# Kernel optimization log

Measured on AMD Instinct MI355X. Metric: run time of the kernel, lower is better.

Reference implementation:

```python
import jax, jax.numpy as jnp
import numpy as np

N_NODES = 100000
N_EDGES = 800000
IN_DIM, HID_DIM, OUT_DIM = 128, 64, 7


def setup_inputs() -> dict:
    key = jax.random.key(0)
    ks = jax.random.split(key, 8)
    x = jax.random.normal(ks[0], (N_NODES, IN_DIM), dtype=jnp.float32)
    edge_index = jax.random.randint(ks[1], (2, N_EDGES), 0, N_NODES, dtype=jnp.int64)
    # Glorot-ish init for weights, zeros for bias (PyG GCNConv default)
    def glorot(k, shape):
        lim = float(np.sqrt(6.0 / (shape[0] + shape[1])))
        return jax.random.uniform(k, shape, dtype=jnp.float32, minval=-lim, maxval=lim)
    return {
        "x": x,
        "edge_index": edge_index,
        "W1": glorot(ks[2], (IN_DIM, HID_DIM)),
        "b1": jnp.zeros((HID_DIM,), jnp.float32),
        "W2": glorot(ks[3], (HID_DIM, HID_DIM)),
        "b2": jnp.zeros((HID_DIM,), jnp.float32),
        "W3": glorot(ks[4], (HID_DIM, OUT_DIM)),
        "b3": jnp.zeros((OUT_DIM,), jnp.float32),
    }


def _gcn_conv(h_in, src, dst, W, b, n_nodes):
    # PyG GCNConv: h = x @ W; add self-loops; D^-1/2 A_hat D^-1/2 aggregation; + b
    h = h_in @ W  # [N, F_out]
    # degree over destination nodes, +1 for self-loop
    deg = jax.ops.segment_sum(jnp.ones_like(dst, dtype=h.dtype), dst,
                              num_segments=n_nodes) + 1.0
    dinv = jax.lax.rsqrt(deg)  # [N]
    coef = dinv[src] * dinv[dst]  # [E]
    msg = h[src] * coef[:, None]  # gather + scale  [E, F_out]
    out = jax.ops.segment_sum(msg, dst, num_segments=n_nodes)  # scatter-add
    out = out + h * (dinv * dinv)[:, None]  # self-loop contribution
    return out + b


def reference(x, edge_index, W1, b1, W2, b2, W3, b3):
    src, dst = edge_index[0], edge_index[1]
    n = x.shape[0]
    h = jax.nn.relu(_gcn_conv(x, src, dst, W1, b1, n))
    # dropout(p=0.5) is identity in eval mode
    h = jax.nn.relu(_gcn_conv(h, src, dst, W2, b2, n))
    return _gcn_conv(h, src, dst, W3, b3, n)
```

## Files before the change

### kernel.cpp

```cpp
#include <hip/hip_runtime.h>

#define N_NODES 100000
#define N_EDGES 800000
#define IN_DIM 128
#define HID 64
#define OUT_DIM 7
#define CAP 32
#define NGROUP 8
#define DSLICE (N_NODES / NGROUP)
#define SUBBLK 390
#define NB_N ((N_NODES + 255) / 256)

typedef __bf16 vbf8 __attribute__((ext_vector_type(8)));
typedef float  vf4  __attribute__((ext_vector_type(4)));

__device__ __forceinline__ void wswz_body(int idx, const float* __restrict__ W,
                                          __bf16* __restrict__ out) {
    int j  = idx & 7;
    int l  = (idx >> 3) & 63;
    int nt = (idx >> 9) & 3;
    int ks = idx >> 11;
    int k  = ks * 32 + ((l >> 4) << 3) + j;
    int n  = nt * 16 + (l & 15);
    out[idx] = (__bf16)W[k * 64 + n];
}

__global__ __launch_bounds__(256)
void k_init(const float* __restrict__ W1, __bf16* __restrict__ Wz1,
            const float* __restrict__ W2, __bf16* __restrict__ Wz2,
            __bf16* __restrict__ HbA, __bf16* __restrict__ HbB,
            float* __restrict__ S) {
    int b = blockIdx.x;
    int t = threadIdx.x;
    if (b < 32) { wswz_body(b * 256 + t, W1, Wz1); return; }
    if (b < 48) { wswz_body((b - 32) * 256 + t, W2, Wz2); return; }
    if (t < 32)       ((unsigned*)(HbA + (size_t)N_NODES * 64))[t] = 0u;
    else if (t < 64)  ((unsigned*)(HbB + (size_t)N_NODES * 64))[t - 32] = 0u;
    else if (t < 71)  S[(size_t)N_NODES * 7 + (t - 64)] = 0.0f;
}

#define GEMM_BLKS ((N_NODES / 16 + 3) / 4)
__global__ __launch_bounds__(256)
void k_gemm1(const float* __restrict__ X, const __bf16* __restrict__ Wswz,
             __bf16* __restrict__ Hb) {
    constexpr int K = IN_DIM, KS = K / 32;
    const int tid = threadIdx.x;
    const int lane = tid & 63;
    const int w = blockIdx.x * 4 + (tid >> 6);
    if (w >= N_NODES / 16) return;
    const int r0 = w * 16;
    const int m = lane & 15;
    const int quad = lane >> 4;

    vbf8 bfrag[KS][4];
    const vbf8* wp = (const vbf8*)Wswz;
    #pragma unroll
    for (int ks = 0; ks < KS; ++ks)
        #pragma unroll
        for (int nt = 0; nt < 4; ++nt)
            bfrag[ks][nt] = wp[(ks * 4 + nt) * 64 + lane];

    vf4 acc[4] = {};
    #pragma unroll
    for (int ks = 0; ks < KS; ++ks) {
        const float* xp = X + (size_t)(r0 + m) * K + ks * 32 + quad * 8;
        float4 f0 = *(const float4*)xp;
        float4 f1 = *(const float4*)(xp + 4);
        vbf8 a;
        a[0] = (__bf16)f0.x; a[1] = (__bf16)f0.y; a[2] = (__bf16)f0.z; a[3] = (__bf16)f0.w;
        a[4] = (__bf16)f1.x; a[5] = (__bf16)f1.y; a[6] = (__bf16)f1.z; a[7] = (__bf16)f1.w;
        #pragma unroll
        for (int nt = 0; nt < 4; ++nt)
            acc[nt] = __builtin_amdgcn_mfma_f32_16x16x32_bf16(a, bfrag[ks][nt], acc[nt], 0, 0, 0);
    }
    #pragma unroll
    for (int nt = 0; nt < 4; ++nt)
        #pragma unroll
        for (int r = 0; r < 4; ++r)
            Hb[(size_t)(r0 + quad * 4 + r) * 64 + nt * 16 + m] = (__bf16)acc[nt][r];
}

#define FILL_BLKS (NGROUP * SUBBLK)
__global__ __launch_bounds__(256)
void k_fill(const int* __restrict__ ei, int* __restrict__ cnt,
            int* __restrict__ csr) {
    int bb = blockIdx.x;
    int group = bb & 7, sub = bb >> 3;
    int lo = group * DSLICE;
    const int4* dst4 = (const int4*)(ei + N_EDGES);
    const int4* src4 = (const int4*)ei;
    for (int e4 = sub * 256 + threadIdx.x; e4 < N_EDGES / 4; e4 += SUBBLK * 256) {
        int4 d4 = dst4[e4];
        bool m0 = (unsigned)(d4.x - lo) < (unsigned)DSLICE;
        bool m1 = (unsigned)(d4.y - lo) < (unsigned)DSLICE;
        bool m2 = (unsigned)(d4.z - lo) < (unsigned)DSLICE;
        bool m3 = (unsigned)(d4.w - lo) < (unsigned)DSLICE;
        if (!(m0 | m1 | m2 | m3)) continue;
        int4 s4 = src4[e4];
        if (m0) { int p = atomicAdd(&cnt[d4.x], 1); if (p < CAP) csr[(size_t)d4.x * CAP + p] = s4.x; }
        if (m1) { int p = atomicAdd(&cnt[d4.y], 1); if (p < CAP) csr[(size_t)d4.y * CAP + p] = s4.y; }
        if (m2) { int p = atomicAdd(&cnt[d4.z], 1); if (p < CAP) csr[(size_t)d4.z * CAP + p] = s4.z; }
        if (m3) { int p = atomicAdd(&cnt[d4.w], 1); if (p < CAP) csr[(size_t)d4.w * CAP + p] = s4.w; }
    }
}

__global__ __launch_bounds__(256)
void k_gather64(const int* __restrict__ cnt, const int* __restrict__ csr,
                const float* __restrict__ bias, const __bf16* __restrict__ Hs,
                __bf16* __restrict__ Ab) {
    int node = blockIdx.x * 32 + (threadIdx.x >> 3);
    int q = threadIdx.x & 7;
    if (node >= N_NODES) return;
    int deg = cnt[node];
    int end = deg < CAP ? deg : CAP;
    float dd = rsqrtf((float)deg + 1.0f);
    vbf8 h8 = *(const vbf8*)(Hs + (size_t)node * 64 + q * 8);
    float acc[8];
    #pragma unroll
    for (int t = 0; t < 8; ++t) acc[t] = (float)h8[t] * dd;

    const int4* row4 = (const int4*)(csr + (size_t)node * CAP);
    int4 qa = row4[0], qb = row4[1], qc = row4[2], qd = row4[3];
    int srcs[16] = {qa.x, qa.y, qa.z, qa.w, qb.x, qb.y, qb.z, qb.w,
                    qc.x, qc.y, qc.z, qc.w, qd.x, qd.y, qd.z, qd.w};
    #pragma unroll
    for (int t = 0; t < 16; ++t) {
        int s = (t < end) ? srcs[t] : N_NODES;
        float ds = rsqrtf((float)cnt[s] + 1.0f);
        vbf8 v = *(const vbf8*)(Hs + (size_t)s * 64 + q * 8);
        #pragma unroll
        for (int u = 0; u < 8; ++u) acc[u] += (float)v[u] * ds;
    }
    for (int j = 16; j < end; ++j) {
        int s = (csr + (size_t)node * CAP)[j];
        float ds = rsqrtf((float)cnt[s] + 1.0f);
        vbf8 v = *(const vbf8*)(Hs + (size_t)s * 64 + q * 8);
        #pragma unroll
        for (int u = 0; u < 8; ++u) acc[u] += (float)v[u] * ds;
    }
    float4 b0 = *(const float4*)(bias + q * 8);
    float4 b1 = *(const float4*)(bias + q * 8 + 4);
    float bb[8] = {b0.x, b0.y, b0.z, b0.w, b1.x, b1.y, b1.z, b1.w};
    vbf8 o;
    #pragma unroll
    for (int t = 0; t < 8; ++t) o[t] = (__bf16)fmaxf(fmaf(acc[t], dd, bb[t]), 0.f);
    *(vbf8*)(Ab + (size_t)node * 64 + q * 8) = o;
}

__global__ __launch_bounds__(256)
void k_gemm2(const __bf16* __restrict__ Ab, const __bf16* __restrict__ Wz2,
             const int* __restrict__ cnt, __bf16* __restrict__ Hb) {
    constexpr int KS = 2;
    const int tid = threadIdx.x;
    const int lane = tid & 63;
    const int w = blockIdx.x * 4 + (tid >> 6);
    if (w >= N_NODES / 16) return;
    const int r0 = w * 16;
    const int m = lane & 15;
    const int quad = lane >> 4;

    vbf8 bfrag[KS][4];
    const vbf8* wp = (const vbf8*)Wz2;
    #pragma unroll
    for (int ks = 0; ks < KS; ++ks)
        #pragma unroll
        for (int nt = 0; nt < 4; ++nt)
            bfrag[ks][nt] = wp[(ks * 4 + nt) * 64 + lane];

    vf4 acc[4] = {};
    #pragma unroll
    for (int ks = 0; ks < KS; ++ks) {
        vbf8 a = *(const vbf8*)(Ab + (size_t)(r0 + m) * 64 + ks * 32 + quad * 8);
        #pragma unroll
        for (int nt = 0; nt < 4; ++nt)
            acc[nt] = __builtin_amdgcn_mfma_f32_16x16x32_bf16(a, bfrag[ks][nt], acc[nt], 0, 0, 0);
    }
    float dv[4];
    #pragma unroll
    for (int r = 0; r < 4; ++r)
        dv[r] = rsqrtf((float)cnt[r0 + quad * 4 + r] + 1.0f);
    #pragma unroll
    for (int nt = 0; nt < 4; ++nt)
        #pragma unroll
        for (int r = 0; r < 4; ++r)
            Hb[(size_t)(r0 + quad * 4 + r) * 64 + nt * 16 + m] = (__bf16)(acc[nt][r] * dv[r]);
}

__global__ __launch_bounds__(256)
void k_gather64m(const int* __restrict__ cnt, const int* __restrict__ csr,
                 const float* __restrict__ bias, const __bf16* __restrict__ Hs,
                 const float* __restrict__ W3, float* __restrict__ S) {
    int node = blockIdx.x * 32 + (threadIdx.x >> 3);
    int q = threadIdx.x & 7;
    if (node >= N_NODES) return;
    int deg = cnt[node];
    int end = deg < CAP ? deg : CAP;
    float dd = rsqrtf((float)deg + 1.0f);
    vbf8 h8 = *(const vbf8*)(Hs + (size_t)node * 64 + q * 8);
    float acc[8];
    #pragma unroll
    for (int t = 0; t < 8; ++t) acc[t] = (float)h8[t];

    const int4* row4 = (const int4*)(csr + (size_t)node * CAP);
    int4 qa = row4[0], qb = row4[1], qc = row4[2], qd = row4[3];
    int srcs[16] = {qa.x, qa.y, qa.z, qa.w, qb.x, qb.y, qb.z, qb.w,
                    qc.x, qc.y, qc.z, qc.w, qd.x, qd.y, qd.z, qd.w};
    #pragma unroll
    for (int t = 0; t < 16; ++t) {
        int s = (t < end) ? srcs[t] : N_NODES;
        vbf8 v = *(const vbf8*)(Hs + (size_t)s * 64 + q * 8);
        #pragma unroll
        for (int u = 0; u < 8; ++u) acc[u] += (float)v[u];
    }
    for (int j = 16; j < end; ++j) {
        int s = (csr + (size_t)node * CAP)[j];
        vbf8 v = *(const vbf8*)(Hs + (size_t)s * 64 + q * 8);
        #pragma unroll
        for (int u = 0; u < 8; ++u) acc[u] += (float)v[u];
    }

    float4 b0 = *(const float4*)(bias + q * 8);
    float4 b1 = *(const float4*)(bias + q * 8 + 4);
    float bb[8] = {b0.x, b0.y, b0.z, b0.w, b1.x, b1.y, b1.z, b1.w};
    float p[7] = {};
    #pragma unroll
    for (int t = 0; t < 8; ++t) {
        float r = fmaxf(fmaf(acc[t], dd, bb[t]), 0.f);
        #pragma unroll
        for (int j = 0; j < 7; ++j)
            p[j] = fmaf(r, W3[(q * 8 + t) * 7 + j], p[j]);
    }
    #pragma unroll
    for (int msk = 1; msk < 8; msk <<= 1)
        #pragma unroll
        for (int j = 0; j < 7; ++j)
            p[j] += __shfl_xor(p[j], msk, 8);
    if (q < 7) {
        float v = p[0];
        if (q == 1) v = p[1]; else if (q == 2) v = p[2]; else if (q == 3) v = p[3];
        else if (q == 4) v = p[4]; else if (q == 5) v = p[5]; else if (q == 6) v = p[6];
        S[(size_t)node * 7 + q] = v * dd;
    }
}

__global__ __launch_bounds__(256)
void k_gather7(const int* __restrict__ cnt, const int* __restrict__ csr,
               const float* __restrict__ S, const float* __restrict__ b3,
               float* __restrict__ Out) {
    int node = blockIdx.x * 32 + (threadIdx.x >> 3);
    int j7 = threadIdx.x & 7;
    if (node >= N_NODES || j7 >= 7) return;
    int deg = cnt[node];
    int end = deg < CAP ? deg : CAP;
    float dd = rsqrtf((float)deg + 1.0f);
    const int4* row4 = (const int4*)(csr + (size_t)node * CAP);
    int4 qa = row4[0], qb = row4[1], qc = row4[2], qd = row4[3];
    int srcs[16] = {qa.x, qa.y, qa.z, qa.w, qb.x, qb.y, qb.z, qb.w,
                    qc.x, qc.y, qc.z, qc.w, qd.x, qd.y, qd.z, qd.w};
    float acc = S[(size_t)node * 7 + j7];
    #pragma unroll
    for (int t = 0; t < 16; ++t) {
        int s = (t < end) ? srcs[t] : N_NODES;
        acc += S[(size_t)s * 7 + j7];
    }
    for (int j = 16; j < end; ++j) {
        int s = (csr + (size_t)node * CAP)[j];
        acc += S[(size_t)s * 7 + j7];
    }
    Out[(size_t)node * 7 + j7] = fmaf(acc, dd, b3[j7]);
}

static inline size_t align256(size_t x) { return (x + 255) & ~(size_t)255; }

extern "C" void kernel_launch(void* const* d_in, const int* in_sizes, int n_in,
                              void* d_out, int out_size, void* d_ws, size_t ws_size,
                              hipStream_t stream) {
    const float* x  = (const float*)d_in[0];
    const int*   ei = (const int*)d_in[1];
    const float* W1 = (const float*)d_in[2];
    const float* b1 = (const float*)d_in[3];
    const float* W2 = (const float*)d_in[4];
    const float* b2 = (const float*)d_in[5];
    const float* W3 = (const float*)d_in[6];
    const float* b3 = (const float*)d_in[7];
    float* out = (float*)d_out;

    char* wsp = (char*)d_ws;
    int*    cnt  = (int*)wsp;    wsp += align256(sizeof(int) * (N_NODES + 1));
    int*    csr  = (int*)wsp;    wsp += align256(sizeof(int) * (size_t)N_NODES * CAP);
    __bf16* Wz1  = (__bf16*)wsp; wsp += align256(sizeof(__bf16) * IN_DIM * 64);
    __bf16* Wz2  = (__bf16*)wsp; wsp += align256(sizeof(__bf16) * HID * 64);
    __bf16* HbA  = (__bf16*)wsp; wsp += align256(sizeof(__bf16) * (size_t)(N_NODES + 1) * 64);
    __bf16* Ab   = (__bf16*)wsp; wsp += align256(sizeof(__bf16) * (size_t)N_NODES * 64);
    __bf16* HbB  = (__bf16*)wsp; wsp += align256(sizeof(__bf16) * (size_t)(N_NODES + 1) * 64);
    float*  bufS = (float*)wsp;  wsp += align256(sizeof(float) * (size_t)(N_NODES + 1) * 7);

    hipMemsetAsync(cnt, 0, sizeof(int) * (N_NODES + 1), stream);
    k_init<<<49, 256, 0, stream>>>(W1, Wz1, W2, Wz2, HbA, HbB, bufS);
    k_gemm1<<<GEMM_BLKS, 256, 0, stream>>>(x, Wz1, HbA);
    k_fill<<<FILL_BLKS, 256, 0, stream>>>(ei, cnt, csr);
    k_gather64<<<N_NODES / 32, 256, 0, stream>>>(cnt, csr, b1, HbA, Ab);
    k_gemm2<<<GEMM_BLKS, 256, 0, stream>>>(Ab, Wz2, cnt, HbB);
    k_gather64m<<<N_NODES / 32, 256, 0, stream>>>(cnt, csr, b2, HbB, W3, bufS);
    k_gather7<<<N_NODES / 32, 256, 0, stream>>>(cnt, csr, bufS, b3, out);
}
```

Baseline: 215.2 us.

## Merge init, gemm1 and fill into one launch; fuse layer-1 gather with gemm2

Combines weight swizzling, the first GEMM (which now reads W1 directly in fp32 and converts it per lane) and the CSR fill into a single kernel whose blocks are split by role. The layer-1 gather now writes its 32-node tile to LDS and runs the second GEMM in the same block, so the Ab intermediate is never written to or read from global memory. This removes two launches and one full round trip of the intermediate activations. In exchange, gemm1 does many more scalar, uncoalesced W1 loads, and the fused kernel adds a block barrier and LDS use.

```diff
diff --git a/kernel.cpp b/kernel.cpp
--- a/kernel.cpp
+++ b/kernel.cpp
@@ -9,10 +9,14 @@
 #define NGROUP 8
 #define DSLICE (N_NODES / NGROUP)
 #define SUBBLK 390
-#define NB_N ((N_NODES + 255) / 256)
 
 typedef __bf16 vbf8 __attribute__((ext_vector_type(8)));
 typedef float  vf4  __attribute__((ext_vector_type(4)));
+
+#define GEMM_BLKS ((N_NODES / 16 + 3) / 4)
+#define FILL_BLKS (NGROUP * SUBBLK)
+#define SWZ2_BLKS 16
+#define PH1_BLKS (GEMM_BLKS + FILL_BLKS + SWZ2_BLKS + 1)
 
 __device__ __forceinline__ void wswz_body(int idx, const float* __restrict__ W,
                                           __bf16* __restrict__ out) {
@@ -25,40 +29,25 @@
     out[idx] = (__bf16)W[k * 64 + n];
 }
 
-__global__ __launch_bounds__(256)
-void k_init(const float* __restrict__ W1, __bf16* __restrict__ Wz1,
-            const float* __restrict__ W2, __bf16* __restrict__ Wz2,
-            __bf16* __restrict__ HbA, __bf16* __restrict__ HbB,
-            float* __restrict__ S) {
-    int b = blockIdx.x;
-    int t = threadIdx.x;
-    if (b < 32) { wswz_body(b * 256 + t, W1, Wz1); return; }
-    if (b < 48) { wswz_body((b - 32) * 256 + t, W2, Wz2); return; }
-    if (t < 32)       ((unsigned*)(HbA + (size_t)N_NODES * 64))[t] = 0u;
-    else if (t < 64)  ((unsigned*)(HbB + (size_t)N_NODES * 64))[t - 32] = 0u;
-    else if (t < 71)  S[(size_t)N_NODES * 7 + (t - 64)] = 0.0f;
-}
-
-#define GEMM_BLKS ((N_NODES / 16 + 3) / 4)
-__global__ __launch_bounds__(256)
-void k_gemm1(const float* __restrict__ X, const __bf16* __restrict__ Wswz,
-             __bf16* __restrict__ Hb) {
+__device__ __forceinline__ void gemm1_body(int g, int tid, const float* __restrict__ X,
+                                           const float* __restrict__ W1,
+                                           __bf16* __restrict__ Hb) {
     constexpr int K = IN_DIM, KS = K / 32;
-    const int tid = threadIdx.x;
     const int lane = tid & 63;
-    const int w = blockIdx.x * 4 + (tid >> 6);
+    const int w = g * 4 + (tid >> 6);
     if (w >= N_NODES / 16) return;
     const int r0 = w * 16;
     const int m = lane & 15;
     const int quad = lane >> 4;
 
     vbf8 bfrag[KS][4];
-    const vbf8* wp = (const vbf8*)Wswz;
     #pragma unroll
     for (int ks = 0; ks < KS; ++ks)
         #pragma unroll
         for (int nt = 0; nt < 4; ++nt)
-            bfrag[ks][nt] = wp[(ks * 4 + nt) * 64 + lane];
+            #pragma unroll
+            for (int j = 0; j < 8; ++j)
+                bfrag[ks][nt][j] = (__bf16)W1[(ks * 32 + quad * 8 + j) * 64 + nt * 16 + m];
 
     vf4 acc[4] = {};
     #pragma unroll
@@ -80,16 +69,13 @@
             Hb[(size_t)(r0 + quad * 4 + r) * 64 + nt * 16 + m] = (__bf16)acc[nt][r];
 }
 
-#define FILL_BLKS (NGROUP * SUBBLK)
-__global__ __launch_bounds__(256)
-void k_fill(const int* __restrict__ ei, int* __restrict__ cnt,
-            int* __restrict__ csr) {
-    int bb = blockIdx.x;
+__device__ __forceinline__ void fill_body(int bb, int tid, const int* __restrict__ ei,
+                                          int* __restrict__ cnt, int* __restrict__ csr) {
     int group = bb & 7, sub = bb >> 3;
     int lo = group * DSLICE;
     const int4* dst4 = (const int4*)(ei + N_EDGES);
     const int4* src4 = (const int4*)ei;
-    for (int e4 = sub * 256 + threadIdx.x; e4 < N_EDGES / 4; e4 += SUBBLK * 256) {
+    for (int e4 = sub * 256 + tid; e4 < N_EDGES / 4; e4 += SUBBLK * 256) {
         int4 d4 = dst4[e4];
         bool m0 = (unsigned)(d4.x - lo) < (unsigned)DSLICE;
         bool m1 = (unsigned)(d4.y - lo) < (unsigned)DSLICE;
@@ -105,12 +91,33 @@
 }
 
 __global__ __launch_bounds__(256)
-void k_gather64(const int* __restrict__ cnt, const int* __restrict__ csr,
+void k_phase1(const int* __restrict__ ei, int* __restrict__ cnt, int* __restrict__ csr,
+              const float* __restrict__ X, const float* __restrict__ W1,
+              const float* __restrict__ W2, __bf16* __restrict__ Wz2,
+              __bf16* __restrict__ HbA, __bf16* __restrict__ HbB,
+              float* __restrict__ S) {
+    int b = blockIdx.x;
+    if (b < GEMM_BLKS) { gemm1_body(b, threadIdx.x, X, W1, HbA); return; }
+    b -= GEMM_BLKS;
+    if (b < FILL_BLKS) { fill_body(b, threadIdx.x, ei, cnt, csr); return; }
+    b -= FILL_BLKS;
+    if (b < SWZ2_BLKS) { wswz_body(b * 256 + threadIdx.x, W2, Wz2); return; }
+    int t = threadIdx.x;
+    if (t < 32)       ((unsigned*)(HbA + (size_t)N_NODES * 64))[t] = 0u;
+    else if (t < 64)  ((unsigned*)(HbB + (size_t)N_NODES * 64))[t - 32] = 0u;
+    else if (t < 71)  S[(size_t)N_NODES * 7 + (t - 64)] = 0.0f;
+}
+
+__global__ __launch_bounds__(256)
+void k_g64gemm2(const int* __restrict__ cnt, const int* __restrict__ csr,
                 const float* __restrict__ bias, const __bf16* __restrict__ Hs,
-                __bf16* __restrict__ Ab) {
-    int node = blockIdx.x * 32 + (threadIdx.x >> 3);
-    int q = threadIdx.x & 7;
-    if (node >= N_NODES) return;
+                const __bf16* __restrict__ Wz2, __bf16* __restrict__ HbB) {
+    __shared__ __bf16 tl[32][72];
+    const int tid = threadIdx.x;
+    const int nl = tid >> 3;
+    const int q  = tid & 7;
+    const int node = blockIdx.x * 32 + nl;
+
     int deg = cnt[node];
     int end = deg < CAP ? deg : CAP;
     float dd = rsqrtf((float)deg + 1.0f);
@@ -144,46 +151,43 @@
     vbf8 o;
     #pragma unroll
     for (int t = 0; t < 8; ++t) o[t] = (__bf16)fmaxf(fmaf(acc[t], dd, bb[t]), 0.f);
-    *(vbf8*)(Ab + (size_t)node * 64 + q * 8) = o;
-}
-
-__global__ __launch_bounds__(256)
-void k_gemm2(const __bf16* __restrict__ Ab, const __bf16* __restrict__ Wz2,
-             const int* __restrict__ cnt, __bf16* __restrict__ Hb) {
-    constexpr int KS = 2;
-    const int tid = threadIdx.x;
+    *(vbf8*)&tl[nl][q * 8] = o;
+    __syncthreads();
+
+    const int wave = tid >> 6;
     const int lane = tid & 63;
-    const int w = blockIdx.x * 4 + (tid >> 6);
-    if (w >= N_NODES / 16) return;
-    const int r0 = w * 16;
     const int m = lane & 15;
     const int quad = lane >> 4;
-
-    vbf8 bfrag[KS][4];
+    const int tile = wave >> 1;
+    const int nt0 = (wave & 1) * 2;
+
+    vbf8 bfrag[2][2];
     const vbf8* wp = (const vbf8*)Wz2;
     #pragma unroll
-    for (int ks = 0; ks < KS; ++ks)
-        #pragma unroll
-        for (int nt = 0; nt < 4; ++nt)
-            bfrag[ks][nt] = wp[(ks * 4 + nt) * 64 + lane];
-
-    vf4 acc[4] = {};
-    #pragma unroll
-    for (int ks = 0; ks < KS; ++ks) {
-        vbf8 a = *(const vbf8*)(Ab + (size_t)(r0 + m) * 64 + ks * 32 + quad * 8);
-        #pragma unroll
-        for (int nt = 0; nt < 4; ++nt)
-            acc[nt] = __builtin_amdgcn_mfma_f32_16x16x32_bf16(a, bfrag[ks][nt], acc[nt], 0, 0, 0);
-    }
+    for (int ks = 0; ks < 2; ++ks)
+        #pragma unroll
+        for (int i = 0; i < 2; ++i)
+            bfrag[ks][i] = wp[(ks * 4 + nt0 + i) * 64 + lane];
+
+    vf4 acc2[2] = {};
+    #pragma unroll
+    for (int ks = 0; ks < 2; ++ks) {
+        vbf8 a = *(const vbf8*)&tl[tile * 16 + m][ks * 32 + quad * 8];
+        #pragma unroll
+        for (int i = 0; i < 2; ++i)
+            acc2[i] = __builtin_amdgcn_mfma_f32_16x16x32_bf16(a, bfrag[ks][i], acc2[i], 0, 0, 0);
+    }
+    const int gr0 = blockIdx.x * 32 + tile * 16;
     float dv[4];
     #pragma unroll
     for (int r = 0; r < 4; ++r)
-        dv[r] = rsqrtf((float)cnt[r0 + quad * 4 + r] + 1.0f);
-    #pragma unroll
-    for (int nt = 0; nt < 4; ++nt)
+        dv[r] = rsqrtf((float)cnt[gr0 + quad * 4 + r] + 1.0f);
+    #pragma unroll
+    for (int i = 0; i < 2; ++i)
         #pragma unroll
         for (int r = 0; r < 4; ++r)
-            Hb[(size_t)(r0 + quad * 4 + r) * 64 + nt * 16 + m] = (__bf16)(acc[nt][r] * dv[r]);
+            HbB[(size_t)(gr0 + quad * 4 + r) * 64 + (nt0 + i) * 16 + m] =
+                (__bf16)(acc2[i][r] * dv[r]);
 }
 
 __global__ __launch_bounds__(256)
@@ -288,19 +292,14 @@
     char* wsp = (char*)d_ws;
     int*    cnt  = (int*)wsp;    wsp += align256(sizeof(int) * (N_NODES + 1));
     int*    csr  = (int*)wsp;    wsp += align256(sizeof(int) * (size_t)N_NODES * CAP);
-    __bf16* Wz1  = (__bf16*)wsp; wsp += align256(sizeof(__bf16) * IN_DIM * 64);
     __bf16* Wz2  = (__bf16*)wsp; wsp += align256(sizeof(__bf16) * HID * 64);
     __bf16* HbA  = (__bf16*)wsp; wsp += align256(sizeof(__bf16) * (size_t)(N_NODES + 1) * 64);
-    __bf16* Ab   = (__bf16*)wsp; wsp += align256(sizeof(__bf16) * (size_t)N_NODES * 64);
     __bf16* HbB  = (__bf16*)wsp; wsp += align256(sizeof(__bf16) * (size_t)(N_NODES + 1) * 64);
     float*  bufS = (float*)wsp;  wsp += align256(sizeof(float) * (size_t)(N_NODES + 1) * 7);
 
     hipMemsetAsync(cnt, 0, sizeof(int) * (N_NODES + 1), stream);
-    k_init<<<49, 256, 0, stream>>>(W1, Wz1, W2, Wz2, HbA, HbB, bufS);
-    k_gemm1<<<GEMM_BLKS, 256, 0, stream>>>(x, Wz1, HbA);
-    k_fill<<<FILL_BLKS, 256, 0, stream>>>(ei, cnt, csr);
-    k_gather64<<<N_NODES / 32, 256, 0, stream>>>(cnt, csr, b1, HbA, Ab);
-    k_gemm2<<<GEMM_BLKS, 256, 0, stream>>>(Ab, Wz2, cnt, HbB);
+    k_phase1<<<PH1_BLKS, 256, 0, stream>>>(ei, cnt, csr, x, W1, W2, Wz2, HbA, HbB, bufS);
+    k_g64gemm2<<<N_NODES / 32, 256, 0, stream>>>(cnt, csr, b1, HbA, Wz2, HbB);
     k_gather64m<<<N_NODES / 32, 256, 0, stream>>>(cnt, csr, b2, HbB, W3, bufS);
     k_gather7<<<N_NODES / 32, 256, 0, stream>>>(cnt, csr, bufS, b3, out);
 }
```

After: 209.2 us. 2.8% less time.
